# Optimization experiments

Measured on AMD Instinct MI355X. Metric: run time of the kernel, lower is better.

## Reference

```python
import jax, jax.numpy as jnp
import numpy as np

B, T, C = 2, 2048, 1024
H = 16
D = C // H  # head_dim = 64


def setup_inputs() -> dict:
    key = jax.random.key(0)
    k1, k2, k3, k4, k5 = jax.random.split(key, 5)
    s = 1.0 / np.sqrt(C)
    return {
        "x": jax.random.normal(k1, (B, T, C), dtype=jnp.float32),
        "w_qkv": jax.random.normal(k2, (C, 3 * C), dtype=jnp.float32) * s,
        "b_qkv": jax.random.normal(k3, (3 * C,), dtype=jnp.float32) * 0.01,
        "w_out": jax.random.normal(k4, (C, C), dtype=jnp.float32) * s,
        "b_out": jax.random.normal(k5, (C,), dtype=jnp.float32) * 0.01,
    }


def reference(x, w_qkv, b_qkv, w_out, b_out):
    Bx, Tx, Cx = x.shape
    qkv = x @ w_qkv + b_qkv                      # [B,T,3C]
    qkv = qkv.reshape(Bx, Tx, 3, H, D)
    q, k, v = qkv[:, :, 0], qkv[:, :, 1], qkv[:, :, 2]  # [B,T,H,D]
    # [B,H,T,T] scores with scaling
    scores = jnp.einsum("bqhd,bkhd->bhqk", q, k) / np.sqrt(D).astype(np.float32)
    causal = jnp.tril(jnp.ones((Tx, Tx), dtype=bool))
    scores = jnp.where(causal[None, None], scores, -jnp.inf)
    attn = jax.nn.softmax(scores, axis=-1)
    out = jnp.einsum("bhqk,bkhd->bqhd", attn, v).reshape(Bx, Tx, Cx)
    return out @ w_out + b_out
```

## Files before the change

### kernel.cpp

```cpp
#include <hip/hip_runtime.h>
#include <stdint.h>

typedef unsigned short u16;
typedef __attribute__((ext_vector_type(8))) short bfrag;
typedef __attribute__((ext_vector_type(4))) short bfrag4;
typedef __attribute__((ext_vector_type(4))) float f32x4;

#define MFMA_BF16 __builtin_amdgcn_mfma_f32_16x16x32_bf16

static constexpr int Bc = 2;
static constexpr int Tc = 2048;
static constexpr int Cc = 1024;
static constexpr int Hc = 16;
static constexpr int Dc = 64;
static constexpr int N3 = 3 * Cc;

__device__ __forceinline__ u16 f2bf(float f) {
    union { unsigned int i; float f; } v; v.f = f;
    unsigned int u = v.i;
    u += 0x7fffu + ((u >> 16) & 1u);
    return (u16)(u >> 16);
}
__device__ __forceinline__ unsigned int fbits(float f) {
    union { unsigned int i; float f; } v; v.f = f; return v.i;
}
__device__ __forceinline__ unsigned int pack_bf2(float hi, float lo) {
    return __builtin_amdgcn_perm(fbits(hi), fbits(lo), 0x07060302u);
}

#if __has_builtin(__builtin_amdgcn_mfma_f32_16x16x16bf16_1k)
__device__ __forceinline__ f32x4 MFMA16(bfrag4 a, bfrag4 b, f32x4 c) {
    return __builtin_amdgcn_mfma_f32_16x16x16bf16_1k(a, b, c, 0, 0, 0);
}
#elif __has_builtin(__builtin_amdgcn_mfma_f32_16x16x16_bf16)
__device__ __forceinline__ f32x4 MFMA16(bfrag4 a, bfrag4 b, f32x4 c) {
    return __builtin_amdgcn_mfma_f32_16x16x16_bf16(a, b, c, 0, 0, 0);
}
#else
__device__ __forceinline__ f32x4 MFMA16(bfrag4 a, bfrag4 b, f32x4 c) {
    bfrag a8 = {a[0], a[1], a[2], a[3], 0, 0, 0, 0};
    bfrag b8 = {b[0], b[1], b[2], b[3], 0, 0, 0, 0};
    return MFMA_BF16(a8, b8, c, 0, 0, 0);
}
#endif

__device__ __forceinline__ void async_load16(const u16* g, u16* lds) {
    __builtin_amdgcn_global_load_lds(
        (const __attribute__((address_space(1))) unsigned int*)g,
        (__attribute__((address_space(3))) unsigned int*)lds, 16, 0, 0);
}

__global__ __launch_bounds__(256) void prep(
    const float* __restrict__ x, const float* __restrict__ w_qkv,
    const float* __restrict__ w_out, u16* __restrict__ xb,
    u16* __restrict__ WqkvT, u16* __restrict__ WoutT) {
    __shared__ u16 tile[32][33];
    const int blk = blockIdx.x, tid = threadIdx.x;
    if (blk < 4096) {
        const int i = (blk * 256 + tid) * 4;
        const float4 v = *(const float4*)(x + i);
        ushort4 o;
        o.x = f2bf(v.x); o.y = f2bf(v.y); o.z = f2bf(v.z); o.w = f2bf(v.w);
        *(ushort4*)(xb + i) = o;
        return;
    }
    const int tx = tid & 31, ty = tid >> 5;
    const float* in; u16* out; int rows, cols, c0, r0;
    if (blk < 4096 + 3072) {
        const int t = blk - 4096;
        in = w_qkv; out = WqkvT; rows = 1024; cols = 3072;
        c0 = (t % 96) * 32; r0 = (t / 96) * 32;
    } else {
        const int t = blk - 7168;
        in = w_out; out = WoutT; rows = 1024; cols = 1024;
        c0 = (t & 31) * 32; r0 = (t >> 5) * 32;
    }
    for (int i = 0; i < 4; i++)
        tile[ty + 8 * i][tx] = f2bf(in[(size_t)(r0 + ty + 8 * i) * cols + c0 + tx]);
    __syncthreads();
    for (int i = 0; i < 4; i++)
        out[(size_t)(c0 + ty + 8 * i) * rows + r0 + tx] = tile[tx][ty + 8 * i];
}

__global__ __launch_bounds__(512, 2) void gemm_qkv(
    const u16* __restrict__ A, const u16* __restrict__ BT,
    const float* __restrict__ bias, u16* __restrict__ outQK,
    u16* __restrict__ Vt, int M, int Nn, int K) {
    extern __shared__ __align__(16) u16 smem[];
    u16* As = smem;
    u16* Bs = smem + 3 * (128 * 32);

    const int tid  = threadIdx.x;
    const int wave = tid >> 6, lane = tid & 63;
    const int quad = lane >> 4, l16 = lane & 15;
    const int wm = wave >> 2, wn = wave & 3;
    const int m0 = blockIdx.y * 128, n0 = blockIdx.x * 384;

    f32x4 acc[4][6];
    #pragma unroll
    for (int i = 0; i < 4; i++)
        #pragma unroll
        for (int j = 0; j < 6; j++)
            acc[i][j] = (f32x4){0.f, 0.f, 0.f, 0.f};

    const int rA = lane >> 2;
    const int cA = ((lane & 3) ^ (rA & 3)) * 8;

    const u16* Ag  = A  + (size_t)(m0 + wave * 16 + rA) * K + cA;
    const u16* Bg0 = BT + (size_t)(n0 + wave * 48 + rA) * K + cA;
    u16* ldsA = As + (wave * 16) * 32;
    u16* ldsB = Bs + (wave * 48) * 32;

    const int swz8 = (quad ^ (l16 & 3)) * 8;
    int offA[4], offB[6];
    #pragma unroll
    for (int mt = 0; mt < 4; mt++)
        offA[mt] = (wm * 64 + mt * 16 + l16) * 32 + swz8;
    #pragma unroll
    for (int nt = 0; nt < 6; nt++)
        offB[nt] = (wn * 96 + nt * 16 + l16) * 32 + swz8;

    #define STAGE_Q(t, bsel)                                                   \
        {                                                                      \
            const int k0_ = (t) << 5;                                          \
            async_load16(Ag + k0_, ldsA + (bsel) * (128 * 32));                \
            _Pragma("unroll")                                                  \
            for (int j = 0; j < 3; j++)                                        \
                async_load16(Bg0 + (size_t)(j * 16) * K + k0_,                 \
                             ldsB + (bsel) * (384 * 32) + j * (16 * 32));      \
        }

    STAGE_Q(0, 0);
    STAGE_Q(1, 1);

    const int T = K >> 5;
    for (int t = 0; t < T; t++) {
        if (t + 1 < T) asm volatile("s_waitcnt vmcnt(4)" ::: "memory");
        else           asm volatile("s_waitcnt vmcnt(0)" ::: "memory");
        __builtin_amdgcn_s_barrier();
        asm volatile("" ::: "memory");
        if (t + 2 < T) { STAGE_Q(t + 2, (t + 2) % 3); }

        const u16* Ab = As + (t % 3) * (128 * 32);
        const u16* Bb = Bs + (t % 3) * (384 * 32);
        bfrag af[4], bf[6];
        #pragma unroll
        for (int mt = 0; mt < 4; mt++) af[mt] = *(const bfrag*)(Ab + offA[mt]);
        #pragma unroll
        for (int nt = 0; nt < 6; nt++) bf[nt] = *(const bfrag*)(Bb + offB[nt]);

        __builtin_amdgcn_s_setprio(1);
        #pragma unroll
        for (int mt = 0; mt < 4; mt++)
            #pragma unroll
            for (int nt = 0; nt < 6; nt++)
                acc[mt][nt] = MFMA_BF16(af[mt], bf[nt], acc[mt][nt], 0, 0, 0);
        __builtin_amdgcn_s_setprio(0);
    }
    #undef STAGE_Q

    #pragma unroll
    for (int nt = 0; nt < 6; nt++) {
        const int gn = n0 + wn * 96 + nt * 16 + l16;
        const float bv = bias[gn];
        if (gn < 2 * Cc) {
            #pragma unroll
            for (int mt = 0; mt < 4; mt++) {
                #pragma unroll
                for (int r = 0; r < 4; r++) {
                    const int gm = m0 + wm * 64 + mt * 16 + quad * 4 + r;
                    outQK[(size_t)gm * Nn + gn] = f2bf(acc[mt][nt][r] + bv);
                }
            }
        } else {
            const int gnv = gn - 2 * Cc;
            const int h = gnv >> 6, d = gnv & 63;
            #pragma unroll
            for (int mt = 0; mt < 4; mt++) {
                const int gmb = m0 + wm * 64 + mt * 16 + quad * 4;
                const int b = gmb >> 11, trow = gmb & (Tc - 1);
                ushort4 o;
                o.x = f2bf(acc[mt][nt][0] + bv);
                o.y = f2bf(acc[mt][nt][1] + bv);
                o.z = f2bf(acc[mt][nt][2] + bv);
                o.w = f2bf(acc[mt][nt][3] + bv);
                *(ushort4*)(Vt + ((size_t)((b * Hc + h) * Dc + d)) * Tc + trow) = o;
            }
        }
    }
}

__global__ __launch_bounds__(512, 2) void gemm_out(
    const u16* __restrict__ A, const u16* __restrict__ BT,
    const float* __restrict__ bias, float* __restrict__ out,
    int M, int Nn, int K) {
    extern __shared__ __align__(16) u16 smem[];
    u16* As = smem;
    u16* Bs = smem + 3 * (128 * 32);

    const int tid  = threadIdx.x;
    const int wave = tid >> 6, lane = tid & 63;
    const int quad = lane >> 4, l16 = lane & 15;
    const int wm = wave >> 2, wn = wave & 3;
    const int m0 = blockIdx.y * 128, n0 = blockIdx.x * 128;

    f32x4 acc[4][2];
    #pragma unroll
    for (int i = 0; i < 4; i++)
        #pragma unroll
        for (int j = 0; j < 2; j++)
            acc[i][j] = (f32x4){0.f, 0.f, 0.f, 0.f};

    const int rA = lane >> 2;
    const int cA = ((lane & 3) ^ (rA & 3)) * 8;

    const u16* Ag = A  + (size_t)(m0 + wave * 16 + rA) * K + cA;
    const u16* Bg = BT + (size_t)(n0 + wave * 16 + rA) * K + cA;
    u16* ldsA = As + (wave * 16) * 32;
    u16* ldsB = Bs + (wave * 16) * 32;

    const int swz8 = (quad ^ (l16 & 3)) * 8;
    int offA[4], offB[2];
    #pragma unroll
    for (int mt = 0; mt < 4; mt++)
        offA[mt] = (wm * 64 + mt * 16 + l16) * 32 + swz8;
    #pragma unroll
    for (int nt = 0; nt < 2; nt++)
        offB[nt] = (wn * 32 + nt * 16 + l16) * 32 + swz8;

    #define STAGE_O(t, bsel)                                                   \
        {                                                                      \
            const int k0_ = (t) << 5;                                          \
            async_load16(Ag + k0_, ldsA + (bsel) * (128 * 32));                \
            async_load16(Bg + k0_, ldsB + (bsel) * (128 * 32));                \
        }

    STAGE_O(0, 0);
    STAGE_O(1, 1);

    const int T = K >> 5;
    for (int t = 0; t < T; t++) {
        if (t + 1 < T) asm volatile("s_waitcnt vmcnt(2)" ::: "memory");
        else           asm volatile("s_waitcnt vmcnt(0)" ::: "memory");
        __builtin_amdgcn_s_barrier();
        asm volatile("" ::: "memory");
        if (t + 2 < T) { STAGE_O(t + 2, (t + 2) % 3); }

        const u16* Ab = As + (t % 3) * (128 * 32);
        const u16* Bb = Bs + (t % 3) * (128 * 32);
        bfrag af[4], bf[2];
        #pragma unroll
        for (int mt = 0; mt < 4; mt++) af[mt] = *(const bfrag*)(Ab + offA[mt]);
        #pragma unroll
        for (int nt = 0; nt < 2; nt++) bf[nt] = *(const bfrag*)(Bb + offB[nt]);

        __builtin_amdgcn_s_setprio(1);
        #pragma unroll
        for (int mt = 0; mt < 4; mt++)
            #pragma unroll
            for (int nt = 0; nt < 2; nt++)
                acc[mt][nt] = MFMA_BF16(af[mt], bf[nt], acc[mt][nt], 0, 0, 0);
        __builtin_amdgcn_s_setprio(0);
    }
    #undef STAGE_O

    #pragma unroll
    for (int nt = 0; nt < 2; nt++) {
        const int gn = n0 + wn * 32 + nt * 16 + l16;
        const float bv = bias[gn];
        #pragma unroll
        for (int mt = 0; mt < 4; mt++) {
            #pragma unroll
            for (int r = 0; r < 4; r++) {
                const int gm = m0 + wm * 64 + mt * 16 + quad * 4 + r;
                out[(size_t)gm * Nn + gn] = acc[mt][nt][r] + bv;
            }
        }
    }
}

__global__ __launch_bounds__(256, 4) void attn_kernel(
    const u16* __restrict__ QKVp, const u16* __restrict__ Vt,
    u16* __restrict__ Ob) {
    __shared__ __align__(16) u16 KsF[2][64 * 64];
    __shared__ __align__(16) u16 VsF[2][64 * 64];

    const int tid  = threadIdx.x;
    const int wave = tid >> 6, lane = tid & 63;
    const int quad = lane >> 4, l16 = lane & 15;

    const int bh = blockIdx.x & 31;
    const int jq = 31 - (blockIdx.x >> 5);
    const int b = bh >> 4, h = bh & 15;
    const u16* Qp = QKVp + (size_t)b * Tc * N3 + h * Dc;
    const u16* Kp = Qp + Cc;
    const u16* Vp = Vt + (size_t)bh * Dc * Tc;

    const int qw = jq * 64 + wave * 16;

    const int row8 = lane >> 3;
    const int swz  = ((lane & 7) ^ row8) * 8;
    const int pk0 = ((quad)     ^ (l16 & 7)) * 8;
    const int pk1 = ((quad + 4) ^ (l16 & 7)) * 8;

    bfrag qf0, qf1;
    {
        const u16* qp = Qp + (size_t)(qw + l16) * N3 + quad * 8;
        qf0 = *(const bfrag*)qp;
        qf1 = *(const bfrag*)(qp + 32);
    }

    float l_i = 0.f;
    f32x4 oacc[4];
    #pragma unroll
    for (int g = 0; g < 4; g++) oacc[g] = (f32x4){0.f, 0.f, 0.f, 0.f};

    #define STAGEKV(t, bsel)                                                    \
        {                                                                       \
            const int k0_ = (t) * 64;                                           \
            _Pragma("unroll")                                                   \
            for (int j = 0; j < 2; j++) {                                       \
                const int rr = wave * 16 + j * 8;                               \
                const int gr = rr + row8;                                       \
                async_load16(Kp + (size_t)(k0_ + gr) * N3 + swz,                \
                             &KsF[bsel][rr * 64]);                              \
                async_load16(Vp + (size_t)gr * Tc + k0_ + swz,                  \
                             &VsF[bsel][rr * 64]);                              \
            }                                                                   \
        }

    STAGEKV(0, 0);
    for (int t = 0; t <= jq; t++) {
        __syncthreads();
        if (t < jq) STAGEKV(t + 1, (t + 1) & 1);
        const u16* Kb = KsF[t & 1];
        const u16* Vb = VsF[t & 1];

        f32x4 s[4];
        __builtin_amdgcn_s_setprio(1);
        #pragma unroll
        for (int g = 0; g < 4; g++) {
            const u16* kb = Kb + (g * 16 + l16) * 64;
            bfrag kf0 = *(const bfrag*)(kb + pk0);
            bfrag kf1 = *(const bfrag*)(kb + pk1);
            f32x4 z = (f32x4){0.f, 0.f, 0.f, 0.f};
            z = MFMA_BF16(kf0, qf0, z, 0, 0, 0);
            z = MFMA_BF16(kf1, qf1, z, 0, 0, 0);
            s[g] = z;
        }
        __builtin_amdgcn_s_setprio(0);

        #pragma unroll
        for (int g = 0; g < 4; g++)
            #pragma unroll
            for (int r = 0; r < 4; r++)
                s[g][r] = __expf(s[g][r] * 0.125f);
        if (t == jq) {
            #pragma unroll
            for (int g = 0; g < 4; g++)
                #pragma unroll
                for (int r = 0; r < 4; r++)
                    if (g * 16 + quad * 4 + r > wave * 16 + l16) s[g][r] = 0.f;
        }
        #pragma unroll
        for (int g = 0; g < 4; g++)
            l_i += s[g][0] + s[g][1] + s[g][2] + s[g][3];

        __builtin_amdgcn_s_setprio(1);
        #pragma unroll
        for (int g = 0; g < 4; g++) {
            union { unsigned int u[2]; bfrag4 v; } pf;
            pf.u[0] = pack_bf2(s[g][1], s[g][0]);
            pf.u[1] = pack_bf2(s[g][3], s[g][2]);
            const int vc = ((2 * g + (quad >> 1)) ^ (l16 & 7)) * 8 + (quad & 1) * 4;
            #pragma unroll
            for (int ng = 0; ng < 4; ng++) {
                const bfrag4 vf = *(const bfrag4*)(Vb + (ng * 16 + l16) * 64 + vc);
                oacc[ng] = MFMA16(vf, pf.v, oacc[ng]);
            }
        }
        __builtin_amdgcn_s_setprio(0);
    }
    #undef STAGEKV

    float rs = l_i;
    rs += __shfl_xor(rs, 16);
    rs += __shfl_xor(rs, 32);
    const float inv = 1.f / rs;
    const int q = qw + l16;
    u16* orow = Ob + (size_t)(b * Tc + q) * Cc + h * Dc + quad * 4;
    #pragma unroll
    for (int ng = 0; ng < 4; ng++) {
        ushort4 o;
        o.x = f2bf(oacc[ng][0] * inv);
        o.y = f2bf(oacc[ng][1] * inv);
        o.z = f2bf(oacc[ng][2] * inv);
        o.w = f2bf(oacc[ng][3] * inv);
        *(ushort4*)(orow + ng * 16) = o;
    }
}

extern "C" void kernel_launch(void* const* d_in, const int* in_sizes, int n_in,
                              void* d_out, int out_size, void* d_ws, size_t ws_size,
                              hipStream_t stream) {
    const float* x     = (const float*)d_in[0];
    const float* w_qkv = (const float*)d_in[1];
    const float* b_qkv = (const float*)d_in[2];
    const float* w_out = (const float*)d_in[3];
    const float* b_out = (const float*)d_in[4];
    float* out = (float*)d_out;
    u16* ws  = (u16*)d_ws;

    u16* xb    = ws;
    u16* WqkvT = xb    + (size_t)4096 * 1024;
    u16* WoutT = WqkvT + (size_t)3072 * 1024;
    u16* QKVp  = WoutT + (size_t)1024 * 1024;
    u16* Vt    = QKVp  + (size_t)4096 * 3072;
    u16* Ao    = xb;

    static bool smem_set = false;
    if (!smem_set) {
        hipFuncSetAttribute(reinterpret_cast<const void*>(gemm_qkv),
                            hipFuncAttributeMaxDynamicSharedMemorySize,
                            96 * 1024);
        hipFuncSetAttribute(reinterpret_cast<const void*>(gemm_out),
                            hipFuncAttributeMaxDynamicSharedMemorySize,
                            48 * 1024);
        smem_set = true;
    }

    prep<<<8192, 256, 0, stream>>>(x, w_qkv, w_out, xb, WqkvT, WoutT);
    gemm_qkv<<<dim3(3072 / 384, 4096 / 128), 512, 96 * 1024, stream>>>(
        xb, WqkvT, b_qkv, QKVp, Vt, 4096, 3072, 1024);
    attn_kernel<<<1024, 256, 0, stream>>>(QKVp, Vt, Ao);
    gemm_out<<<dim3(1024 / 128, 4096 / 128), 512, 48 * 1024, stream>>>(
        Ao, WoutT, b_out, out, 4096, 1024, 1024);
}
```

Before: 177.7 us.

## Process two query tiles per attention block to reuse staged K/V tiles

Each attention workgroup now handles 128 query rows, as two 64-row halves each wave owns 16 rows of, instead of 64. Every K/V tile staged in shared memory feeds both query halves, which halves the global K/V traffic and the number of blocks (512 instead of 1024). The exponential switches to exp2f with a pre-folded log2e scale, the setprio hints are dropped, and launch bounds drop to 2 waves per SIMD to make room for the doubled accumulators. The cost is higher register pressure, fewer blocks for load balancing across CUs, and the last tile running with only one half active.

```diff
diff --git a/kernel.cpp b/kernel.cpp
--- a/kernel.cpp
+++ b/kernel.cpp
@@ -279,7 +279,7 @@
     }
 }
 
-__global__ __launch_bounds__(256, 4) void attn_kernel(
+__global__ __launch_bounds__(256, 2) void attn_kernel(
     const u16* __restrict__ QKVp, const u16* __restrict__ Vt,
     u16* __restrict__ Ob) {
     __shared__ __align__(16) u16 KsF[2][64 * 64];
@@ -290,30 +290,36 @@
     const int quad = lane >> 4, l16 = lane & 15;
 
     const int bh = blockIdx.x & 31;
-    const int jq = 31 - (blockIdx.x >> 5);
+    const int jq = 15 - (blockIdx.x >> 5);
     const int b = bh >> 4, h = bh & 15;
     const u16* Qp = QKVp + (size_t)b * Tc * N3 + h * Dc;
     const u16* Kp = Qp + Cc;
     const u16* Vp = Vt + (size_t)bh * Dc * Tc;
 
-    const int qw = jq * 64 + wave * 16;
+    const int qbase = jq * 128 + wave * 16;
 
     const int row8 = lane >> 3;
     const int swz  = ((lane & 7) ^ row8) * 8;
     const int pk0 = ((quad)     ^ (l16 & 7)) * 8;
     const int pk1 = ((quad + 4) ^ (l16 & 7)) * 8;
 
-    bfrag qf0, qf1;
+    bfrag qfA0, qfA1, qfB0, qfB1;
     {
-        const u16* qp = Qp + (size_t)(qw + l16) * N3 + quad * 8;
-        qf0 = *(const bfrag*)qp;
-        qf1 = *(const bfrag*)(qp + 32);
-    }
-
-    float l_i = 0.f;
-    f32x4 oacc[4];
-    #pragma unroll
-    for (int g = 0; g < 4; g++) oacc[g] = (f32x4){0.f, 0.f, 0.f, 0.f};
+        const u16* qpA = Qp + (size_t)(qbase + l16) * N3 + quad * 8;
+        qfA0 = *(const bfrag*)qpA;
+        qfA1 = *(const bfrag*)(qpA + 32);
+        const u16* qpB = qpA + (size_t)64 * N3;
+        qfB0 = *(const bfrag*)qpB;
+        qfB1 = *(const bfrag*)(qpB + 32);
+    }
+
+    float lA = 0.f, lB = 0.f;
+    f32x4 oA[4], oB[4];
+    #pragma unroll
+    for (int g = 0; g < 4; g++) {
+        oA[g] = (f32x4){0.f, 0.f, 0.f, 0.f};
+        oB[g] = (f32x4){0.f, 0.f, 0.f, 0.f};
+    }
 
     #define STAGEKV(t, bsel)                                                    \
         {                                                                       \
@@ -329,74 +335,111 @@
             }                                                                   \
         }
 
+    const int NT = 2 * jq + 2;
+    const float SCL2 = 0.125f * 1.44269504f;
+
     STAGEKV(0, 0);
-    for (int t = 0; t <= jq; t++) {
+    for (int t = 0; t < NT; t++) {
         __syncthreads();
-        if (t < jq) STAGEKV(t + 1, (t + 1) & 1);
+        if (t + 1 < NT) STAGEKV(t + 1, (t + 1) & 1);
         const u16* Kb = KsF[t & 1];
         const u16* Vb = VsF[t & 1];
 
-        f32x4 s[4];
-        __builtin_amdgcn_s_setprio(1);
+        const bool doA = (t + 1 < NT);
+        f32x4 sA[4], sB[4];
         #pragma unroll
         for (int g = 0; g < 4; g++) {
             const u16* kb = Kb + (g * 16 + l16) * 64;
             bfrag kf0 = *(const bfrag*)(kb + pk0);
             bfrag kf1 = *(const bfrag*)(kb + pk1);
             f32x4 z = (f32x4){0.f, 0.f, 0.f, 0.f};
-            z = MFMA_BF16(kf0, qf0, z, 0, 0, 0);
-            z = MFMA_BF16(kf1, qf1, z, 0, 0, 0);
-            s[g] = z;
-        }
-        __builtin_amdgcn_s_setprio(0);
+            z = MFMA_BF16(kf0, qfB0, z, 0, 0, 0);
+            z = MFMA_BF16(kf1, qfB1, z, 0, 0, 0);
+            sB[g] = z;
+            if (doA) {
+                f32x4 y = (f32x4){0.f, 0.f, 0.f, 0.f};
+                y = MFMA_BF16(kf0, qfA0, y, 0, 0, 0);
+                y = MFMA_BF16(kf1, qfA1, y, 0, 0, 0);
+                sA[g] = y;
+            }
+        }
 
         #pragma unroll
         for (int g = 0; g < 4; g++)
             #pragma unroll
             for (int r = 0; r < 4; r++)
-                s[g][r] = __expf(s[g][r] * 0.125f);
-        if (t == jq) {
+                sB[g][r] = exp2f(sB[g][r] * SCL2);
+        if (doA) {
             #pragma unroll
             for (int g = 0; g < 4; g++)
                 #pragma unroll
                 for (int r = 0; r < 4; r++)
-                    if (g * 16 + quad * 4 + r > wave * 16 + l16) s[g][r] = 0.f;
-        }
-        #pragma unroll
-        for (int g = 0; g < 4; g++)
-            l_i += s[g][0] + s[g][1] + s[g][2] + s[g][3];
-
-        __builtin_amdgcn_s_setprio(1);
+                    sA[g][r] = exp2f(sA[g][r] * SCL2);
+        }
+        if (t >= 2 * jq) {
+            const int kq = wave * 16 + l16;
+            if (doA) {
+                #pragma unroll
+                for (int g = 0; g < 4; g++)
+                    #pragma unroll
+                    for (int r = 0; r < 4; r++)
+                        if (g * 16 + quad * 4 + r > kq) sA[g][r] = 0.f;
+            } else {
+                #pragma unroll
+                for (int g = 0; g < 4; g++)
+                    #pragma unroll
+                    for (int r = 0; r < 4; r++)
+                        if (g * 16 + quad * 4 + r > kq) sB[g][r] = 0.f;
+            }
+        }
         #pragma unroll
         for (int g = 0; g < 4; g++) {
-            union { unsigned int u[2]; bfrag4 v; } pf;
-            pf.u[0] = pack_bf2(s[g][1], s[g][0]);
-            pf.u[1] = pack_bf2(s[g][3], s[g][2]);
+            lB += sB[g][0] + sB[g][1] + sB[g][2] + sB[g][3];
+            if (doA) lA += sA[g][0] + sA[g][1] + sA[g][2] + sA[g][3];
+        }
+
+        #pragma unroll
+        for (int g = 0; g < 4; g++) {
+            union { unsigned int u[2]; bfrag4 v; } pfB, pfA;
+            pfB.u[0] = pack_bf2(sB[g][1], sB[g][0]);
+            pfB.u[1] = pack_bf2(sB[g][3], sB[g][2]);
+            if (doA) {
+                pfA.u[0] = pack_bf2(sA[g][1], sA[g][0]);
+                pfA.u[1] = pack_bf2(sA[g][3], sA[g][2]);
+            }
             const int vc = ((2 * g + (quad >> 1)) ^ (l16 & 7)) * 8 + (quad & 1) * 4;
             #pragma unroll
             for (int ng = 0; ng < 4; ng++) {
                 const bfrag4 vf = *(const bfrag4*)(Vb + (ng * 16 + l16) * 64 + vc);
-                oacc[ng] = MFMA16(vf, pf.v, oacc[ng]);
-            }
-        }
-        __builtin_amdgcn_s_setprio(0);
+                oB[ng] = MFMA16(vf, pfB.v, oB[ng]);
+                if (doA) oA[ng] = MFMA16(vf, pfA.v, oA[ng]);
+            }
+        }
     }
     #undef STAGEKV
 
-    float rs = l_i;
-    rs += __shfl_xor(rs, 16);
-    rs += __shfl_xor(rs, 32);
-    const float inv = 1.f / rs;
-    const int q = qw + l16;
-    u16* orow = Ob + (size_t)(b * Tc + q) * Cc + h * Dc + quad * 4;
+    float rsA = lA, rsB = lB;
+    rsA += __shfl_xor(rsA, 16); rsA += __shfl_xor(rsA, 32);
+    rsB += __shfl_xor(rsB, 16); rsB += __shfl_xor(rsB, 32);
+    const float invA = 1.f / rsA;
+    const float invB = 1.f / rsB;
+    const int qA = qbase + l16;
+    u16* orowA = Ob + (size_t)(b * Tc + qA) * Cc + h * Dc + quad * 4;
+    u16* orowB = orowA + (size_t)64 * Cc;
     #pragma unroll
     for (int ng = 0; ng < 4; ng++) {
         ushort4 o;
-        o.x = f2bf(oacc[ng][0] * inv);
-        o.y = f2bf(oacc[ng][1] * inv);
-        o.z = f2bf(oacc[ng][2] * inv);
-        o.w = f2bf(oacc[ng][3] * inv);
-        *(ushort4*)(orow + ng * 16) = o;
+        o.x = f2bf(oA[ng][0] * invA);
+        o.y = f2bf(oA[ng][1] * invA);
+        o.z = f2bf(oA[ng][2] * invA);
+        o.w = f2bf(oA[ng][3] * invA);
+        *(ushort4*)(orowA + ng * 16) = o;
+        ushort4 p;
+        p.x = f2bf(oB[ng][0] * invB);
+        p.y = f2bf(oB[ng][1] * invB);
+        p.z = f2bf(oB[ng][2] * invB);
+        p.w = f2bf(oB[ng][3] * invB);
+        *(ushort4*)(orowB + ng * 16) = p;
     }
 }
 
@@ -432,7 +475,7 @@
     prep<<<8192, 256, 0, stream>>>(x, w_qkv, w_out, xb, WqkvT, WoutT);
     gemm_qkv<<<dim3(3072 / 384, 4096 / 128), 512, 96 * 1024, stream>>>(
         xb, WqkvT, b_qkv, QKVp, Vt, 4096, 3072, 1024);
-    attn_kernel<<<1024, 256, 0, stream>>>(QKVp, Vt, Ao);
+    attn_kernel<<<512, 256, 0, stream>>>(QKVp, Vt, Ao);
     gemm_out<<<dim3(1024 / 128, 4096 / 128), 512, 48 * 1024, stream>>>(
         Ao, WoutT, b_out, out, 4096, 1024, 1024);
 }
```

New measurement: 220.0 us. +23.8%, slower.
